# Kernel tuning notes

Measured on AMD Instinct MI355X. Metric: run time of the kernel, lower is better.

## Reference

```python
import jax, jax.numpy as jnp
import numpy as np

N, E = 50000, 800000
H, C = 4, 32          # heads, per-head channels (hidden_channels)
IN, ED, OUT = 128, 16, 16
HC = H * C            # 128
NEG_SLOPE = 0.2


def _add_self_loops(edge_index, edge_attr, n):
    # PyG default add_self_loops=True with fill_value='mean' for edge_attr
    src, dst = edge_index[0], edge_index[1]
    loop = jnp.arange(n, dtype=edge_index.dtype)
    cnt = jax.ops.segment_sum(jnp.ones_like(dst, dtype=edge_attr.dtype), dst, num_segments=n)
    sums = jax.ops.segment_sum(edge_attr, dst, num_segments=n)
    loop_attr = sums / jnp.maximum(cnt, 1.0)[:, None]
    src = jnp.concatenate([src, loop])
    dst = jnp.concatenate([dst, loop])
    eattr = jnp.concatenate([edge_attr, loop_attr], axis=0)
    return src, dst, eattr


def _gatv2_layer(x, src, dst, eattr, Wl, bl, Wr, br, We, att, bias, n):
    # x: [n, F_in]; out: [n, H*C]
    xl = (x @ Wl + bl).reshape(n, H, C)   # source transform
    xr = (x @ Wr + br).reshape(n, H, C)   # destination transform
    e = (eattr @ We).reshape(-1, H, C)    # edge transform
    m = xl[src] + xr[dst] + e             # [E', H, C] per-edge message pre-activation
    s = jnp.einsum('ehc,hc->eh', jax.nn.leaky_relu(m, NEG_SLOPE), att)
    # segment softmax over destination nodes (self-loops guarantee nonempty segments)
    smax = jax.ops.segment_max(s, dst, num_segments=n)
    ex = jnp.exp(s - smax[dst])
    denom = jax.ops.segment_sum(ex, dst, num_segments=n)
    alpha = ex / denom[dst]               # [E', H]
    out = jax.ops.segment_sum(alpha[:, :, None] * xl[src], dst, num_segments=n)
    return out.reshape(n, HC) + bias


def setup_inputs() -> dict:
    key = jax.random.key(0)
    ks = jax.random.split(key, 20)
    g = lambda k, shape, fan: jax.random.normal(k, shape, jnp.float32) * (1.0 / np.sqrt(fan))
    inp = {
        'x': jax.random.normal(ks[0], (N, IN), jnp.float32),
        'edge_index': jax.random.randint(ks[1], (2, E), 0, N, jnp.int32),
        'edge_attr': jax.random.normal(ks[2], (E, ED), jnp.float32),
        # conv1 params
        'Wl1': g(ks[3], (IN, HC), IN), 'bl1': jnp.zeros((HC,), jnp.float32),
        'Wr1': g(ks[4], (IN, HC), IN), 'br1': jnp.zeros((HC,), jnp.float32),
        'We1': g(ks[5], (ED, HC), ED),
        'att1': g(ks[6], (H, C), C),
        'bias1': jnp.zeros((HC,), jnp.float32),
        # conv2 params (input is HC)
        'Wl2': g(ks[7], (HC, HC), HC), 'bl2': jnp.zeros((HC,), jnp.float32),
        'Wr2': g(ks[8], (HC, HC), HC), 'br2': jnp.zeros((HC,), jnp.float32),
        'We2': g(ks[9], (ED, HC), ED),
        'att2': g(ks[10], (H, C), C),
        'bias2': jnp.zeros((HC,), jnp.float32),
        # final linear
        'Wlin': g(ks[11], (HC, OUT), HC),
        'blin': jnp.zeros((OUT,), jnp.float32),
    }
    return inp


def reference(x, edge_index, edge_attr,
              Wl1, bl1, Wr1, br1, We1, att1, bias1,
              Wl2, bl2, Wr2, br2, We2, att2, bias2,
              Wlin, blin):
    # eval mode: F.dropout(p=0.6, training=False) is identity
    src, dst, eattr = _add_self_loops(edge_index, edge_attr, N)
    h = _gatv2_layer(x, src, dst, eattr, Wl1, bl1, Wr1, br1, We1, att1, bias1, N)
    h = jax.nn.elu(h)
    h = _gatv2_layer(h, src, dst, eattr, Wl2, bl2, Wr2, br2, We2, att2, bias2, N)
    return h @ Wlin + blin
```

## Files before the change

### kernel.cpp

```cpp
#include <hip/hip_runtime.h>
#include <math.h>

#define HC 128
#define ED 16
#define OUT_F 16
#define NEG 0.2f

#define RFL(x) __builtin_amdgcn_readfirstlane(x)


__global__ __launch_bounds__(256) void k_count(const int* __restrict__ ei, int* __restrict__ deg, int E) {
  int e = blockIdx.x * 256 + threadIdx.x;
  if (e < E) atomicAdd(&deg[ei[E + e]], 1);
}

__global__ __launch_bounds__(256) void k_scan_local(const int* __restrict__ deg, int* __restrict__ loc,
                                                    int* __restrict__ bsum, int n) {
  int tid = threadIdx.x, lane = tid & 63, w = tid >> 6;
  int base = blockIdx.x * 1024 + tid * 4;
  int v0 = (base + 0 < n) ? deg[base + 0] + 1 : 0;
  int v1 = (base + 1 < n) ? deg[base + 1] + 1 : 0;
  int v2 = (base + 2 < n) ? deg[base + 2] + 1 : 0;
  int v3 = (base + 3 < n) ? deg[base + 3] + 1 : 0;
  int s4 = v0 + v1 + v2 + v3;
  int sc = s4;
  #pragma unroll
  for (int off = 1; off < 64; off <<= 1) {
    int t = __shfl_up(sc, off);
    if (lane >= off) sc += t;
  }
  __shared__ int ws[4];
  if (lane == 63) ws[w] = sc;
  __syncthreads();
  int woff = 0;
  for (int j = 0; j < w; j++) woff += ws[j];
  int excl = woff + sc - s4;
  if (base + 0 < n) loc[base + 0] = excl + v0;
  if (base + 1 < n) loc[base + 1] = excl + v0 + v1;
  if (base + 2 < n) loc[base + 2] = excl + v0 + v1 + v2;
  if (base + 3 < n) loc[base + 3] = excl + v0 + v1 + v2 + v3;
  if (tid == 255) bsum[blockIdx.x] = ws[0] + ws[1] + ws[2] + ws[3];
}

__global__ __launch_bounds__(64) void k_scan_bsum(int* __restrict__ bsum, int B) {
  int lane = threadIdx.x;
  int carry = 0;
  for (int base = 0; base < B; base += 64) {
    int i = base + lane;
    int v = (i < B) ? bsum[i] : 0;
    int sc = v;
    #pragma unroll
    for (int off = 1; off < 64; off <<= 1) {
      int t = __shfl_up(sc, off);
      if (lane >= off) sc += t;
    }
    if (i < B) bsum[i] = carry + sc - v;
    carry += __shfl(sc, 63);
  }
}

__global__ __launch_bounds__(256) void k_scan_write(const int* __restrict__ loc, const int* __restrict__ bsum,
                                                    int* __restrict__ rowptr, int n) {
  int i = blockIdx.x * 256 + threadIdx.x;
  if (i < n) rowptr[i + 1] = loc[i] + bsum[i >> 10];
  if (i == 0) rowptr[0] = 0;
}

__global__ __launch_bounds__(256) void k_scatter(const int* __restrict__ ei, const int* __restrict__ rowptr,
                                                 int* __restrict__ fill, int* __restrict__ eid,
                                                 int* __restrict__ esrc, int E, int Etot) {
  int e = blockIdx.x * 256 + threadIdx.x;
  if (e >= Etot) return;
  int src, dst;
  if (e < E) { src = ei[e]; dst = ei[E + e]; }
  else       { src = dst = e - E; }
  int pos = rowptr[dst] + atomicAdd(&fill[dst], 1);
  eid[pos] = e;
  esrc[pos] = src;
}

__global__ __launch_bounds__(256) void k_loop_attr(const int* __restrict__ rowptr, const int* __restrict__ eid,
                                                   const float* __restrict__ eattr, float* __restrict__ la,
                                                   int n, int E) {
  int t = blockIdx.x * 256 + threadIdx.x;
  if (t >= n * ED) return;
  int node = t >> 4, k = t & 15;
  int r0 = rowptr[node], d = rowptr[node + 1] - r0;
  float sum = 0.f;
  for (int i = 0; i < d; i++) {
    int e = eid[r0 + i];
    if (e < E) sum += eattr[(size_t)e * ED + k];
  }
  int cnt = d - 1;
  if (cnt < 1) cnt = 1;
  la[t] = sum / (float)cnt;
}


#define COMP(v, j) ((j) == 0 ? (v).x : (j) == 1 ? (v).y : (j) == 2 ? (v).z : (v).w)

__global__ __launch_bounds__(256) void k_gemm128(const float* __restrict__ X, const float* __restrict__ W,
                                                 const float* __restrict__ bias, float* __restrict__ out, int nrows) {
  __shared__ float Ws[HC * HC];
  for (int i = threadIdx.x * 4; i < HC * HC; i += 256 * 4)
    *(float4*)&Ws[i] = *(const float4*)&W[i];
  __syncthreads();
  int lane = threadIdx.x & 63;
  int gw = RFL(blockIdx.x * 4 + (threadIdx.x >> 6));
  int nw = gridDim.x * 4;
  float b0 = bias[2 * lane], b1 = bias[2 * lane + 1];
  for (int r0 = gw * 4; r0 < nrows; r0 += nw * 4) {
    float a00 = b0, a01 = b1, a10 = b0, a11 = b1, a20 = b0, a21 = b1, a30 = b0, a31 = b1;
    int nr = nrows - r0; if (nr > 4) nr = 4;
    if (nr == 4) {
      for (int k4 = 0; k4 < 32; k4++) {
        float4 x0 = *(const float4*)&X[(size_t)(r0 + 0) * HC + k4 * 4];
        float4 x1 = *(const float4*)&X[(size_t)(r0 + 1) * HC + k4 * 4];
        float4 x2 = *(const float4*)&X[(size_t)(r0 + 2) * HC + k4 * 4];
        float4 x3 = *(const float4*)&X[(size_t)(r0 + 3) * HC + k4 * 4];
        #pragma unroll
        for (int j = 0; j < 4; j++) {
          float2 wv = *(const float2*)&Ws[(k4 * 4 + j) * HC + 2 * lane];
          a00 += COMP(x0, j) * wv.x; a01 += COMP(x0, j) * wv.y;
          a10 += COMP(x1, j) * wv.x; a11 += COMP(x1, j) * wv.y;
          a20 += COMP(x2, j) * wv.x; a21 += COMP(x2, j) * wv.y;
          a30 += COMP(x3, j) * wv.x; a31 += COMP(x3, j) * wv.y;
        }
      }
      *(float2*)&out[(size_t)(r0 + 0) * HC + 2 * lane] = make_float2(a00, a01);
      *(float2*)&out[(size_t)(r0 + 1) * HC + 2 * lane] = make_float2(a10, a11);
      *(float2*)&out[(size_t)(r0 + 2) * HC + 2 * lane] = make_float2(a20, a21);
      *(float2*)&out[(size_t)(r0 + 3) * HC + 2 * lane] = make_float2(a30, a31);
    } else {
      for (int r = 0; r < nr; r++) {
        float c0 = b0, c1 = b1;
        for (int k = 0; k < HC; k++) {
          float xv = X[(size_t)(r0 + r) * HC + k];
          float2 wv = *(const float2*)&Ws[k * HC + 2 * lane];
          c0 += xv * wv.x; c1 += xv * wv.y;
        }
        *(float2*)&out[(size_t)(r0 + r) * HC + 2 * lane] = make_float2(c0, c1);
      }
    }
  }
}


#define WE_DOT(mv0, mv1, c0, c1, c2, c3)            \
  mv0 += c0.x * w0[0];  mv1 += c0.x * w1[0];        \
  mv0 += c0.y * w0[1];  mv1 += c0.y * w1[1];        \
  mv0 += c0.z * w0[2];  mv1 += c0.z * w1[2];        \
  mv0 += c0.w * w0[3];  mv1 += c0.w * w1[3];        \
  mv0 += c1.x * w0[4];  mv1 += c1.x * w1[4];        \
  mv0 += c1.y * w0[5];  mv1 += c1.y * w1[5];        \
  mv0 += c1.z * w0[6];  mv1 += c1.z * w1[6];        \
  mv0 += c1.w * w0[7];  mv1 += c1.w * w1[7];        \
  mv0 += c2.x * w0[8];  mv1 += c2.x * w1[8];        \
  mv0 += c2.y * w0[9];  mv1 += c2.y * w1[9];        \
  mv0 += c2.z * w0[10]; mv1 += c2.z * w1[10];       \
  mv0 += c2.w * w0[11]; mv1 += c2.w * w1[11];       \
  mv0 += c3.x * w0[12]; mv1 += c3.x * w1[12];       \
  mv0 += c3.y * w0[13]; mv1 += c3.y * w1[13];       \
  mv0 += c3.z * w0[14]; mv1 += c3.z * w1[14];       \
  mv0 += c3.w * w0[15]; mv1 += c3.w * w1[15];

__global__ __launch_bounds__(256) void k_layer(const float* __restrict__ xl, const float* __restrict__ xr,
                                               const int* __restrict__ rowptr, const int* __restrict__ eid,
                                               const int* __restrict__ esrc, const float* __restrict__ eattr,
                                               const float* __restrict__ la, const float* __restrict__ We,
                                               const float* __restrict__ att, const float* __restrict__ bias,
                                               float* __restrict__ out, int elu, int n, int E) {
  int lane = threadIdx.x & 63;
  int gw = RFL(blockIdx.x * 4 + (threadIdx.x >> 6));
  int nw = gridDim.x * 4;
  float a0 = att[2 * lane], a1 = att[2 * lane + 1];
  float b0 = bias[2 * lane], b1 = bias[2 * lane + 1];
  float w0[ED], w1[ED];
  #pragma unroll
  for (int k = 0; k < ED; k++) {
    float2 wv = *(const float2*)&We[k * HC + 2 * lane];
    w0[k] = wv.x; w1[k] = wv.y;
  }
  for (int node = gw; node < n; node += nw) {
    int r0 = RFL(rowptr[node]);
    int deg = RFL(rowptr[node + 1]) - r0;
    float2 xrv = *(const float2*)&xr[(size_t)node * HC + 2 * lane];
    float m = -INFINITY, l = 0.f, acc0 = 0.f, acc1 = 0.f;
    int eA = RFL(eid[r0]), sA = RFL(esrc[r0]);
    int eB = 0, sB = 0;
    if (deg > 1) { eB = RFL(eid[r0 + 1]); sB = RFL(esrc[r0 + 1]); }
    int i = 0;
    for (; i + 2 <= deg; i += 2) {
      const float* eaA = (eA < E) ? &eattr[(size_t)eA * ED] : &la[(size_t)(eA - E) * ED];
      const float* eaB = (eB < E) ? &eattr[(size_t)eB * ED] : &la[(size_t)(eB - E) * ED];
      float4 cA0 = *(const float4*)&eaA[0];
      float4 cA1 = *(const float4*)&eaA[4];
      float4 cA2 = *(const float4*)&eaA[8];
      float4 cA3 = *(const float4*)&eaA[12];
      float4 cB0 = *(const float4*)&eaB[0];
      float4 cB1 = *(const float4*)&eaB[4];
      float4 cB2 = *(const float4*)&eaB[8];
      float4 cB3 = *(const float4*)&eaB[12];
      float2 xA = *(const float2*)&xl[(size_t)sA * HC + 2 * lane];
      float2 xB = *(const float2*)&xl[(size_t)sB * HC + 2 * lane];
      int nxt = i + 2;
      if (nxt < deg)     { eA = RFL(eid[r0 + nxt]);     sA = RFL(esrc[r0 + nxt]); }
      if (nxt + 1 < deg) { eB = RFL(eid[r0 + nxt + 1]); sB = RFL(esrc[r0 + nxt + 1]); }
      float mA0 = xA.x + xrv.x, mA1 = xA.y + xrv.y;
      float mB0 = xB.x + xrv.x, mB1 = xB.y + xrv.y;
      WE_DOT(mA0, mA1, cA0, cA1, cA2, cA3)
      WE_DOT(mB0, mB1, cB0, cB1, cB2, cB3)
      float lA0 = mA0 > 0.f ? mA0 : NEG * mA0;
      float lA1 = mA1 > 0.f ? mA1 : NEG * mA1;
      float lB0 = mB0 > 0.f ? mB0 : NEG * mB0;
      float lB1 = mB1 > 0.f ? mB1 : NEG * mB1;
      float cA = lA0 * a0 + lA1 * a1;
      float cB = lB0 * a0 + lB1 * a1;
      cA += __shfl_xor(cA, 1);  cB += __shfl_xor(cB, 1);
      cA += __shfl_xor(cA, 2);  cB += __shfl_xor(cB, 2);
      cA += __shfl_xor(cA, 4);  cB += __shfl_xor(cB, 4);
      cA += __shfl_xor(cA, 8);  cB += __shfl_xor(cB, 8);
      float newm = fmaxf(m, fmaxf(cA, cB));
      float scale = __expf(m - newm);
      float pA = __expf(cA - newm);
      float pB = __expf(cB - newm);
      l = l * scale + pA + pB;
      acc0 = acc0 * scale + pA * xA.x + pB * xB.x;
      acc1 = acc1 * scale + pA * xA.y + pB * xB.y;
      m = newm;
    }
    if (i < deg) {
      const float* ea = (eA < E) ? &eattr[(size_t)eA * ED] : &la[(size_t)(eA - E) * ED];
      float4 c0 = *(const float4*)&ea[0];
      float4 c1 = *(const float4*)&ea[4];
      float4 c2 = *(const float4*)&ea[8];
      float4 c3 = *(const float4*)&ea[12];
      float2 xA = *(const float2*)&xl[(size_t)sA * HC + 2 * lane];
      float m0 = xA.x + xrv.x, m1 = xA.y + xrv.y;
      WE_DOT(m0, m1, c0, c1, c2, c3)
      float l0 = m0 > 0.f ? m0 : NEG * m0;
      float l1 = m1 > 0.f ? m1 : NEG * m1;
      float c = l0 * a0 + l1 * a1;
      c += __shfl_xor(c, 1);
      c += __shfl_xor(c, 2);
      c += __shfl_xor(c, 4);
      c += __shfl_xor(c, 8);
      float newm = fmaxf(m, c);
      float scale = __expf(m - newm);
      float p = __expf(c - newm);
      l = l * scale + p;
      acc0 = acc0 * scale + p * xA.x;
      acc1 = acc1 * scale + p * xA.y;
      m = newm;
    }
    float rl = 1.0f / l;
    float o0 = acc0 * rl + b0;
    float o1 = acc1 * rl + b1;
    if (elu) {
      o0 = o0 > 0.f ? o0 : (expf(o0) - 1.f);
      o1 = o1 > 0.f ? o1 : (expf(o1) - 1.f);
    }
    *(float2*)&out[(size_t)node * HC + 2 * lane] = make_float2(o0, o1);
  }
}


__global__ __launch_bounds__(256) void k_final(const float* __restrict__ h2, const float* __restrict__ Wlin,
                                               const float* __restrict__ blin, float* __restrict__ out, int n) {
  int t = blockIdx.x * 256 + threadIdx.x;
  if (t >= n * OUT_F) return;
  int node = t >> 4, o = t & 15;
  float acc = blin[o];
  const float* hp = &h2[(size_t)node * HC];
  #pragma unroll 4
  for (int k = 0; k < HC; k++) acc += hp[k] * Wlin[k * OUT_F + o];
  out[t] = acc;
}


extern "C" void kernel_launch(void* const* d_in, const int* in_sizes, int n_in,
                              void* d_out, int out_size, void* d_ws, size_t ws_size,
                              hipStream_t stream) {
  const float* x     = (const float*)d_in[0];
  const int*   ei    = (const int*)d_in[1];
  const float* eattr = (const float*)d_in[2];
  const float* Wl1 = (const float*)d_in[3];  const float* bl1 = (const float*)d_in[4];
  const float* Wr1 = (const float*)d_in[5];  const float* br1 = (const float*)d_in[6];
  const float* We1 = (const float*)d_in[7];  const float* att1 = (const float*)d_in[8];
  const float* bias1 = (const float*)d_in[9];
  const float* Wl2 = (const float*)d_in[10]; const float* bl2 = (const float*)d_in[11];
  const float* Wr2 = (const float*)d_in[12]; const float* br2 = (const float*)d_in[13];
  const float* We2 = (const float*)d_in[14]; const float* att2 = (const float*)d_in[15];
  const float* bias2 = (const float*)d_in[16];
  const float* Wlin = (const float*)d_in[17]; const float* blin = (const float*)d_in[18];
  float* out = (float*)d_out;

  const int N = in_sizes[0] / HC;
  const int E = in_sizes[1] / 2;
  const int Etot = E + N;
  const int NB = (N + 1023) / 1024;

  char* w = (char*)d_ws;
  size_t off = 0;
  auto alloc = [&](size_t b) { size_t o = off; off += (b + 255) & ~(size_t)255; return o; };
  float* xl   = (float*)(w + alloc((size_t)N * HC * 4));
  float* xr   = (float*)(w + alloc((size_t)N * HC * 4));
  float* hbuf = (float*)(w + alloc((size_t)N * HC * 4));
  float* la   = (float*)(w + alloc((size_t)N * ED * 4));
  int* rowptr = (int*)(w + alloc((size_t)(N + 1) * 4));
  int* eid    = (int*)(w + alloc((size_t)Etot * 4));
  int* esrc   = (int*)(w + alloc((size_t)Etot * 4));
  int* deg    = (int*)(w + alloc((size_t)N * 4));
  int* loc    = (int*)(w + alloc((size_t)N * 4));
  int* bsum   = (int*)(w + alloc((size_t)NB * 4));

  hipMemsetAsync(deg, 0, (size_t)N * 4, stream);
  k_count<<<(E + 255) / 256, 256, 0, stream>>>(ei, deg, E);
  k_scan_local<<<NB, 256, 0, stream>>>(deg, loc, bsum, N);
  k_scan_bsum<<<1, 64, 0, stream>>>(bsum, NB);
  k_scan_write<<<(N + 255) / 256, 256, 0, stream>>>(loc, bsum, rowptr, N);
  hipMemsetAsync(deg, 0, (size_t)N * 4, stream);
  k_scatter<<<(Etot + 255) / 256, 256, 0, stream>>>(ei, rowptr, deg, eid, esrc, E, Etot);
  k_loop_attr<<<(N * ED + 255) / 256, 256, 0, stream>>>(rowptr, eid, eattr, la, N, E);

  int gemm_blocks = (N + 15) / 16;
  int layer_blocks = (N + 3) / 4;

  k_gemm128<<<gemm_blocks, 256, 0, stream>>>(x, Wl1, bl1, xl, N);
  k_gemm128<<<gemm_blocks, 256, 0, stream>>>(x, Wr1, br1, xr, N);
  k_layer<<<layer_blocks, 256, 0, stream>>>(xl, xr, rowptr, eid, esrc, eattr, la, We1, att1, bias1, hbuf, 1, N, E);

  k_gemm128<<<gemm_blocks, 256, 0, stream>>>(hbuf, Wl2, bl2, xl, N);
  k_gemm128<<<gemm_blocks, 256, 0, stream>>>(hbuf, Wr2, br2, xr, N);
  k_layer<<<layer_blocks, 256, 0, stream>>>(xl, xr, rowptr, eid, esrc, eattr, la, We2, att2, bias2, hbuf, 0, N, E);

  k_final<<<(N * OUT_F + 255) / 256, 256, 0, stream>>>(hbuf, Wlin, blin, out, N);
}
```

Before: 692.9 us.

## Compute self-loop edge term from accumulated edge projections, drop loop_attr kernel

```diff
diff --git a/kernel.cpp b/kernel.cpp
--- a/kernel.cpp
+++ b/kernel.cpp
@@ -18,10 +18,10 @@
                                                     int* __restrict__ bsum, int n) {
   int tid = threadIdx.x, lane = tid & 63, w = tid >> 6;
   int base = blockIdx.x * 1024 + tid * 4;
-  int v0 = (base + 0 < n) ? deg[base + 0] + 1 : 0;
-  int v1 = (base + 1 < n) ? deg[base + 1] + 1 : 0;
-  int v2 = (base + 2 < n) ? deg[base + 2] + 1 : 0;
-  int v3 = (base + 3 < n) ? deg[base + 3] + 1 : 0;
+  int v0 = (base + 0 < n) ? deg[base + 0] : 0;
+  int v1 = (base + 1 < n) ? deg[base + 1] : 0;
+  int v2 = (base + 2 < n) ? deg[base + 2] : 0;
+  int v3 = (base + 3 < n) ? deg[base + 3] : 0;
   int s4 = v0 + v1 + v2 + v3;
   int sc = s4;
   #pragma unroll
@@ -67,33 +67,12 @@
 }
 
 __global__ __launch_bounds__(256) void k_scatter(const int* __restrict__ ei, const int* __restrict__ rowptr,
-                                                 int* __restrict__ fill, int* __restrict__ eid,
-                                                 int* __restrict__ esrc, int E, int Etot) {
+                                                 int* __restrict__ fill, int2* __restrict__ epk, int E) {
   int e = blockIdx.x * 256 + threadIdx.x;
-  if (e >= Etot) return;
-  int src, dst;
-  if (e < E) { src = ei[e]; dst = ei[E + e]; }
-  else       { src = dst = e - E; }
+  if (e >= E) return;
+  int src = ei[e], dst = ei[E + e];
   int pos = rowptr[dst] + atomicAdd(&fill[dst], 1);
-  eid[pos] = e;
-  esrc[pos] = src;
-}
-
-__global__ __launch_bounds__(256) void k_loop_attr(const int* __restrict__ rowptr, const int* __restrict__ eid,
-                                                   const float* __restrict__ eattr, float* __restrict__ la,
-                                                   int n, int E) {
-  int t = blockIdx.x * 256 + threadIdx.x;
-  if (t >= n * ED) return;
-  int node = t >> 4, k = t & 15;
-  int r0 = rowptr[node], d = rowptr[node + 1] - r0;
-  float sum = 0.f;
-  for (int i = 0; i < d; i++) {
-    int e = eid[r0 + i];
-    if (e < E) sum += eattr[(size_t)e * ED + k];
-  }
-  int cnt = d - 1;
-  if (cnt < 1) cnt = 1;
-  la[t] = sum / (float)cnt;
+  epk[pos] = make_int2(e, src);
 }
 
 
@@ -165,11 +144,10 @@
   mv0 += c3.w * w0[15]; mv1 += c3.w * w1[15];
 
 __global__ __launch_bounds__(256) void k_layer(const float* __restrict__ xl, const float* __restrict__ xr,
-                                               const int* __restrict__ rowptr, const int* __restrict__ eid,
-                                               const int* __restrict__ esrc, const float* __restrict__ eattr,
-                                               const float* __restrict__ la, const float* __restrict__ We,
+                                               const int* __restrict__ rowptr, const int2* __restrict__ epk,
+                                               const float* __restrict__ eattr, const float* __restrict__ We,
                                                const float* __restrict__ att, const float* __restrict__ bias,
-                                               float* __restrict__ out, int elu, int n, int E) {
+                                               float* __restrict__ out, int elu, int n) {
   int lane = threadIdx.x & 63;
   int gw = RFL(blockIdx.x * 4 + (threadIdx.x >> 6));
   int nw = gridDim.x * 4;
@@ -183,16 +161,17 @@
   }
   for (int node = gw; node < n; node += nw) {
     int r0 = RFL(rowptr[node]);
-    int deg = RFL(rowptr[node + 1]) - r0;
+    int degO = RFL(rowptr[node + 1]) - r0;
     float2 xrv = *(const float2*)&xr[(size_t)node * HC + 2 * lane];
     float m = -INFINITY, l = 0.f, acc0 = 0.f, acc1 = 0.f;
-    int eA = RFL(eid[r0]), sA = RFL(esrc[r0]);
-    int eB = 0, sB = 0;
-    if (deg > 1) { eB = RFL(eid[r0 + 1]); sB = RFL(esrc[r0 + 1]); }
+    float sd0 = 0.f, sd1 = 0.f;
+    int eA = 0, sA = 0, eB = 0, sB = 0;
+    if (degO > 0) { int2 p = epk[r0];     eA = RFL(p.x); sA = RFL(p.y); }
+    if (degO > 1) { int2 p = epk[r0 + 1]; eB = RFL(p.x); sB = RFL(p.y); }
     int i = 0;
-    for (; i + 2 <= deg; i += 2) {
-      const float* eaA = (eA < E) ? &eattr[(size_t)eA * ED] : &la[(size_t)(eA - E) * ED];
-      const float* eaB = (eB < E) ? &eattr[(size_t)eB * ED] : &la[(size_t)(eB - E) * ED];
+    for (; i + 2 <= degO; i += 2) {
+      const float* eaA = &eattr[(size_t)eA * ED];
+      const float* eaB = &eattr[(size_t)eB * ED];
       float4 cA0 = *(const float4*)&eaA[0];
       float4 cA1 = *(const float4*)&eaA[4];
       float4 cA2 = *(const float4*)&eaA[8];
@@ -204,12 +183,15 @@
       float2 xA = *(const float2*)&xl[(size_t)sA * HC + 2 * lane];
       float2 xB = *(const float2*)&xl[(size_t)sB * HC + 2 * lane];
       int nxt = i + 2;
-      if (nxt < deg)     { eA = RFL(eid[r0 + nxt]);     sA = RFL(esrc[r0 + nxt]); }
-      if (nxt + 1 < deg) { eB = RFL(eid[r0 + nxt + 1]); sB = RFL(esrc[r0 + nxt + 1]); }
-      float mA0 = xA.x + xrv.x, mA1 = xA.y + xrv.y;
-      float mB0 = xB.x + xrv.x, mB1 = xB.y + xrv.y;
-      WE_DOT(mA0, mA1, cA0, cA1, cA2, cA3)
-      WE_DOT(mB0, mB1, cB0, cB1, cB2, cB3)
+      if (nxt < degO)     { int2 p = epk[r0 + nxt];     eA = RFL(p.x); sA = RFL(p.y); }
+      if (nxt + 1 < degO) { int2 p = epk[r0 + nxt + 1]; eB = RFL(p.x); sB = RFL(p.y); }
+      float dA0 = 0.f, dA1 = 0.f, dB0 = 0.f, dB1 = 0.f;
+      WE_DOT(dA0, dA1, cA0, cA1, cA2, cA3)
+      WE_DOT(dB0, dB1, cB0, cB1, cB2, cB3)
+      sd0 += dA0 + dB0;
+      sd1 += dA1 + dB1;
+      float mA0 = dA0 + xA.x + xrv.x, mA1 = dA1 + xA.y + xrv.y;
+      float mB0 = dB0 + xB.x + xrv.x, mB1 = dB1 + xB.y + xrv.y;
       float lA0 = mA0 > 0.f ? mA0 : NEG * mA0;
       float lA1 = mA1 > 0.f ? mA1 : NEG * mA1;
       float lB0 = mB0 > 0.f ? mB0 : NEG * mB0;
@@ -229,15 +211,17 @@
       acc1 = acc1 * scale + pA * xA.y + pB * xB.y;
       m = newm;
     }
-    if (i < deg) {
-      const float* ea = (eA < E) ? &eattr[(size_t)eA * ED] : &la[(size_t)(eA - E) * ED];
+    if (i < degO) {
+      const float* ea = &eattr[(size_t)eA * ED];
       float4 c0 = *(const float4*)&ea[0];
       float4 c1 = *(const float4*)&ea[4];
       float4 c2 = *(const float4*)&ea[8];
       float4 c3 = *(const float4*)&ea[12];
       float2 xA = *(const float2*)&xl[(size_t)sA * HC + 2 * lane];
-      float m0 = xA.x + xrv.x, m1 = xA.y + xrv.y;
-      WE_DOT(m0, m1, c0, c1, c2, c3)
+      float d0 = 0.f, d1 = 0.f;
+      WE_DOT(d0, d1, c0, c1, c2, c3)
+      sd0 += d0; sd1 += d1;
+      float m0 = d0 + xA.x + xrv.x, m1 = d1 + xA.y + xrv.y;
       float l0 = m0 > 0.f ? m0 : NEG * m0;
       float l1 = m1 > 0.f ? m1 : NEG * m1;
       float c = l0 * a0 + l1 * a1;
@@ -251,6 +235,26 @@
       l = l * scale + p;
       acc0 = acc0 * scale + p * xA.x;
       acc1 = acc1 * scale + p * xA.y;
+      m = newm;
+    }
+    {
+      float2 xS = *(const float2*)&xl[(size_t)node * HC + 2 * lane];
+      float inv_cnt = 1.0f / (float)(degO > 0 ? degO : 1);
+      float m0 = sd0 * inv_cnt + xS.x + xrv.x;
+      float m1 = sd1 * inv_cnt + xS.y + xrv.y;
+      float l0 = m0 > 0.f ? m0 : NEG * m0;
+      float l1 = m1 > 0.f ? m1 : NEG * m1;
+      float c = l0 * a0 + l1 * a1;
+      c += __shfl_xor(c, 1);
+      c += __shfl_xor(c, 2);
+      c += __shfl_xor(c, 4);
+      c += __shfl_xor(c, 8);
+      float newm = fmaxf(m, c);
+      float scale = __expf(m - newm);
+      float p = __expf(c - newm);
+      l = l * scale + p;
+      acc0 = acc0 * scale + p * xS.x;
+      acc1 = acc1 * scale + p * xS.y;
       m = newm;
     }
     float rl = 1.0f / l;
@@ -297,7 +301,6 @@
 
   const int N = in_sizes[0] / HC;
   const int E = in_sizes[1] / 2;
-  const int Etot = E + N;
   const int NB = (N + 1023) / 1024;
 
   char* w = (char*)d_ws;
@@ -306,10 +309,8 @@
   float* xl   = (float*)(w + alloc((size_t)N * HC * 4));
   float* xr   = (float*)(w + alloc((size_t)N * HC * 4));
   float* hbuf = (float*)(w + alloc((size_t)N * HC * 4));
-  float* la   = (float*)(w + alloc((size_t)N * ED * 4));
   int* rowptr = (int*)(w + alloc((size_t)(N + 1) * 4));
-  int* eid    = (int*)(w + alloc((size_t)Etot * 4));
-  int* esrc   = (int*)(w + alloc((size_t)Etot * 4));
+  int2* epk   = (int2*)(w + alloc((size_t)E * 8));
   int* deg    = (int*)(w + alloc((size_t)N * 4));
   int* loc    = (int*)(w + alloc((size_t)N * 4));
   int* bsum   = (int*)(w + alloc((size_t)NB * 4));
@@ -320,19 +321,18 @@
   k_scan_bsum<<<1, 64, 0, stream>>>(bsum, NB);
   k_scan_write<<<(N + 255) / 256, 256, 0, stream>>>(loc, bsum, rowptr, N);
   hipMemsetAsync(deg, 0, (size_t)N * 4, stream);
-  k_scatter<<<(Etot + 255) / 256, 256, 0, stream>>>(ei, rowptr, deg, eid, esrc, E, Etot);
-  k_loop_attr<<<(N * ED + 255) / 256, 256, 0, stream>>>(rowptr, eid, eattr, la, N, E);
+  k_scatter<<<(E + 255) / 256, 256, 0, stream>>>(ei, rowptr, deg, epk, E);
 
   int gemm_blocks = (N + 15) / 16;
   int layer_blocks = (N + 3) / 4;
 
   k_gemm128<<<gemm_blocks, 256, 0, stream>>>(x, Wl1, bl1, xl, N);
   k_gemm128<<<gemm_blocks, 256, 0, stream>>>(x, Wr1, br1, xr, N);
-  k_layer<<<layer_blocks, 256, 0, stream>>>(xl, xr, rowptr, eid, esrc, eattr, la, We1, att1, bias1, hbuf, 1, N, E);
+  k_layer<<<layer_blocks, 256, 0, stream>>>(xl, xr, rowptr, epk, eattr, We1, att1, bias1, hbuf, 1, N);
 
   k_gemm128<<<gemm_blocks, 256, 0, stream>>>(hbuf, Wl2, bl2, xl, N);
   k_gemm128<<<gemm_blocks, 256, 0, stream>>>(hbuf, Wr2, br2, xr, N);
-  k_layer<<<layer_blocks, 256, 0, stream>>>(xl, xr, rowptr, eid, esrc, eattr, la, We2, att2, bias2, hbuf, 0, N, E);
+  k_layer<<<layer_blocks, 256, 0, stream>>>(xl, xr, rowptr, epk, eattr, We2, att2, bias2, hbuf, 0, N);
 
   k_final<<<(N * OUT_F + 255) / 256, 256, 0, stream>>>(hbuf, Wlin, blin, out, N);
 }
```

New measurement: 664.8 us. -4.1%, faster.
